# Optimization experiments

Hardware: AMD Instinct MI355X
Metric: run time of the kernel (lower is better)

The kernel has to match this reference:

```python
import jax, jax.numpy as jnp
import numpy as np

N, E, G = 100000, 1600000, 128
IN, HID, HEADS, EDIM, OUT = 16, 32, 4, 8, 4
HC = HEADS * HID


def _p(k, shape):
    return jax.random.normal(k, shape, jnp.float32) * 0.1


def setup_inputs():
    key = jax.random.key(0)
    ks = list(jax.random.split(key, 24))
    nxt = iter(ks)
    d = dict(
        x=jax.random.normal(next(nxt), (N, IN), jnp.float32),
        edge_index=jax.random.randint(next(nxt), (2, E), 0, N),
        edge_attr=jax.random.normal(next(nxt), (E, EDIM), jnp.float32),
        batch=jnp.sort(jax.random.randint(next(nxt), (N,), 0, G)),
    )
    # conv1: in=IN -> heads*hid
    d['wl1'] = _p(next(nxt), (IN, HC));  d['bl1'] = jnp.zeros((HC,), jnp.float32)
    d['wr1'] = _p(next(nxt), (IN, HC));  d['br1'] = jnp.zeros((HC,), jnp.float32)
    d['we1'] = _p(next(nxt), (EDIM, HC)); d['att1'] = _p(next(nxt), (HEADS, HID)); d['bc1'] = jnp.zeros((HC,), jnp.float32)
    # conv2: in=HC -> heads*hid
    d['wl2'] = _p(next(nxt), (HC, HC));  d['bl2'] = jnp.zeros((HC,), jnp.float32)
    d['wr2'] = _p(next(nxt), (HC, HC));  d['br2'] = jnp.zeros((HC,), jnp.float32)
    d['we2'] = _p(next(nxt), (EDIM, HC)); d['att2'] = _p(next(nxt), (HEADS, HID)); d['bc2'] = jnp.zeros((HC,), jnp.float32)
    # conv3: in=HC -> 1*hid (heads=1)
    d['wl3'] = _p(next(nxt), (HC, HID)); d['bl3'] = jnp.zeros((HID,), jnp.float32)
    d['wr3'] = _p(next(nxt), (HC, HID)); d['br3'] = jnp.zeros((HID,), jnp.float32)
    d['we3'] = _p(next(nxt), (EDIM, HID)); d['att3'] = _p(next(nxt), (1, HID)); d['bc3'] = jnp.zeros((HID,), jnp.float32)
    d['w_fc1'] = _p(next(nxt), (HID, 2 * HID)); d['b_fc1'] = jnp.zeros((2 * HID,), jnp.float32)
    d['w_fc2'] = _p(next(nxt), (2 * HID, OUT)); d['b_fc2'] = jnp.zeros((OUT,), jnp.float32)
    return d


def _gatv2(x, src, dst, eattr, wl, bl, wr, br, we, att, bias, n):
    # PyG GATv2Conv: e_ij = a^T . leaky_relu(Wl x_j + Wr x_i + We e_ij)
    H, C = att.shape
    xl = (x @ wl + bl).reshape(-1, H, C)  # source transform [N,H,C]
    xr = (x @ wr + br).reshape(-1, H, C)  # target transform [N,H,C]
    ea = (eattr @ we).reshape(-1, H, C)   # edge transform   [E,H,C]
    e = jax.nn.leaky_relu(xl[src] + xr[dst] + ea, 0.2)  # [E,H,C]
    logit = jnp.einsum('ehc,hc->eh', e, att)            # [E,H]
    m = jax.ops.segment_max(logit, dst, num_segments=n)
    p = jnp.exp(logit - m[dst])
    s = jax.ops.segment_sum(p, dst, num_segments=n)
    alpha = p / (s[dst] + 1e-16)                        # segment softmax per dst
    out = jax.ops.segment_sum(xl[src] * alpha[:, :, None], dst, num_segments=n)
    return out.reshape(n, H * C) + bias


def reference(x, edge_index, edge_attr, batch,
              wl1, bl1, wr1, br1, we1, att1, bc1,
              wl2, bl2, wr2, br2, we2, att2, bc2,
              wl3, bl3, wr3, br3, we3, att3, bc3,
              w_fc1, b_fc1, w_fc2, b_fc2):
    n = x.shape[0]
    src, dst = edge_index[0], edge_index[1]
    # add_self_loops=True with fill_value='mean' (mean of incoming edge_attr per node)
    ones_e = jnp.ones((src.shape[0],), x.dtype)
    cnt = jax.ops.segment_sum(ones_e, dst, num_segments=n)
    loop_attr = jax.ops.segment_sum(edge_attr, dst, num_segments=n) / jnp.maximum(cnt, 1.0)[:, None]
    ar = jnp.arange(n)
    src_a = jnp.concatenate([src, ar])
    dst_a = jnp.concatenate([dst, ar])
    ea = jnp.concatenate([edge_attr, loop_attr], axis=0)

    h = jax.nn.elu(_gatv2(x, src_a, dst_a, ea, wl1, bl1, wr1, br1, we1, att1, bc1, n))
    h = jax.nn.elu(_gatv2(h, src_a, dst_a, ea, wl2, bl2, wr2, br2, we2, att2, bc2, n))
    h = jax.nn.elu(_gatv2(h, src_a, dst_a, ea, wl3, bl3, wr3, br3, we3, att3, bc3, n))

    # global mean pool over graphs
    gs = jax.ops.segment_sum(h, batch, num_segments=G)
    gc = jax.ops.segment_sum(jnp.ones((n,), h.dtype), batch, num_segments=G)
    g = gs / jnp.maximum(gc, 1.0)[:, None]

    g = jax.nn.elu(g @ w_fc1 + b_fc1)
    return g @ w_fc2 + b_fc2
```

## Files before the change

### kernel.cpp

```cpp
#include <hip/hip_runtime.h>
#include <cstdint>
#include <type_traits>

constexpr int GNUM = 128;
constexpr int DBINS = 64;

typedef _Float16 h2 __attribute__((ext_vector_type(2)));
typedef _Float16 h4 __attribute__((ext_vector_type(4)));
typedef _Float16 h8 __attribute__((ext_vector_type(8)));
typedef float f4 __attribute__((ext_vector_type(4)));


__global__ __launch_bounds__(256) void hist_kernel(const int* __restrict__ dst,
                                                   int* __restrict__ cnt, int E) {
  int i = blockIdx.x * 256 + threadIdx.x;
  if (i < E) atomicAdd(&cnt[dst[i]], 1);
}

__global__ __launch_bounds__(256) void scan_part_kernel(const int* __restrict__ cnt,
                                                        int* __restrict__ bpart,
                                                        int* __restrict__ deghist, int n) {
  __shared__ int red[256];
  __shared__ int dh[DBINS];
  int base = blockIdx.x * 512;
  int t = threadIdx.x;
  if (t < DBINS) dh[t] = 0;
  __syncthreads();
  int s = 0;
  int i0 = base + t, i1 = base + 256 + t;
  if (i0 < n) { int c = cnt[i0] + 1; s += c; atomicAdd(&dh[c < DBINS - 1 ? c : DBINS - 1], 1); }
  if (i1 < n) { int c = cnt[i1] + 1; s += c; atomicAdd(&dh[c < DBINS - 1 ? c : DBINS - 1], 1); }
  red[t] = s;
  __syncthreads();
  for (int off = 128; off > 0; off >>= 1) {
    if (t < off) red[t] += red[t + off];
    __syncthreads();
  }
  if (t == 0) bpart[blockIdx.x] = red[0];
  if (t < DBINS && dh[t] > 0) atomicAdd(&deghist[t], dh[t]);
}

__global__ __launch_bounds__(1024) void scan_top_kernel(const int* __restrict__ bpart,
                                                        int* __restrict__ boff,
                                                        int* __restrict__ row_ptr,
                                                        const int* __restrict__ batch,
                                                        int* __restrict__ gstart,
                                                        const int* __restrict__ deghist,
                                                        int* __restrict__ degbase,
                                                        int B, int n) {
  __shared__ int buf[1024];
  __shared__ int dsc[DBINS];
  int t = threadIdx.x;
  buf[t] = (t < B) ? bpart[t] : 0;
  __syncthreads();
  for (int off = 1; off < 1024; off <<= 1) {
    int v = (t >= off) ? buf[t - off] : 0;
    __syncthreads();
    buf[t] += v;
    __syncthreads();
  }
  if (t < B) boff[t] = (t == 0) ? 0 : buf[t - 1];
  if (t == 0) row_ptr[n] = buf[1023];
  if (t <= GNUM) {
    int lo = 0, hi = n;
    while (lo < hi) {
      int mid = (lo + hi) >> 1;
      if (batch[mid] < t) lo = mid + 1; else hi = mid;
    }
    gstart[t] = lo;
  }
  int myc = 0;
  if (t < DBINS) { myc = deghist[t]; dsc[t] = myc; }
  __syncthreads();
  for (int off = 1; off < DBINS; off <<= 1) {
    int v = (t >= off && t < DBINS) ? dsc[t - off] : 0;
    __syncthreads();
    if (t < DBINS) dsc[t] += v;
    __syncthreads();
  }
  if (t < DBINS) degbase[t] = dsc[t] - myc;
}

__global__ __launch_bounds__(256) void scan_write_kernel(const int* __restrict__ cnt,
                                                         const int* __restrict__ boff,
                                                         int* __restrict__ row_ptr,
                                                         int* __restrict__ fill, int n) {
  __shared__ int red[256];
  int base = blockIdx.x * 512;
  int t = threadIdx.x;
  int i0 = base + 2 * t, i1 = base + 2 * t + 1;
  int v0 = (i0 < n) ? cnt[i0] + 1 : 0;
  int v1 = (i1 < n) ? cnt[i1] + 1 : 0;
  int val = v0 + v1;
  red[t] = val;
  __syncthreads();
  for (int off = 1; off < 256; off <<= 1) {
    int u = (t >= off) ? red[t - off] : 0;
    __syncthreads();
    red[t] += u;
    __syncthreads();
  }
  int o = boff[blockIdx.x] + red[t] - val;
  if (i0 < n) { row_ptr[i0] = o; fill[i0] = o; }
  if (i1 < n) { row_ptr[i1] = o + v0; fill[i1] = o + v0; }
}

__global__ __launch_bounds__(256) void permute_kernel(const int* __restrict__ cnt,
                                                      int* __restrict__ degbase,
                                                      int* __restrict__ perm, int n) {
  __shared__ int lcnt[DBINS];
  __shared__ int lbase[DBINS];
  int t = threadIdx.x;
  if (t < DBINS) lcnt[t] = 0;
  __syncthreads();
  int i = blockIdx.x * 256 + t;
  int bin = 0, lr = 0;
  if (i < n) {
    int c = cnt[i] + 1;
    bin = c < DBINS - 1 ? c : DBINS - 1;
    lr = atomicAdd(&lcnt[bin], 1);
  }
  __syncthreads();
  if (t < DBINS && lcnt[t] > 0) lbase[t] = atomicAdd(&degbase[t], lcnt[t]);
  __syncthreads();
  if (i < n) perm[lbase[bin] + lr] = i;
}

__global__ __launch_bounds__(256) void scatter_kernel(const int* __restrict__ src,
                                                      const int* __restrict__ dst,
                                                      const float* __restrict__ ea,
                                                      int* __restrict__ fill,
                                                      int* __restrict__ csr_src,
                                                      _Float16* __restrict__ ea_csr, int E) {
  int i = blockIdx.x * 256 + threadIdx.x;
  if (i >= E) return;
  int d = dst[i];
  int p = atomicAdd(&fill[d], 1);
  csr_src[p] = src[i];
  float4 e0 = *(const float4*)&ea[(size_t)i * 8];
  float4 e1 = *(const float4*)&ea[(size_t)i * 8 + 4];
  h8 v;
  v[0] = (_Float16)e0.x; v[1] = (_Float16)e0.y; v[2] = (_Float16)e0.z; v[3] = (_Float16)e0.w;
  v[4] = (_Float16)e1.x; v[5] = (_Float16)e1.y; v[6] = (_Float16)e1.z; v[7] = (_Float16)e1.w;
  *(h8*)&ea_csr[(size_t)p * 8] = v;
}

__global__ __launch_bounds__(256) void selfloop_kernel(const int* __restrict__ row_ptr,
                                                       int* __restrict__ csr_src,
                                                       _Float16* __restrict__ ea_csr, int n) {
  int idx = blockIdx.x * 256 + threadIdx.x;
  int i = idx >> 3, c = idx & 7;
  if (i >= n) return;
  int s = row_ptr[i], e = row_ptr[i + 1] - 1;
  float a = 0.f;
  for (int j = s; j < e; j++) a += (float)ea_csr[(size_t)j * 8 + c];
  float inv = 1.f / fmaxf((float)(e - s), 1.f);
  ea_csr[(size_t)e * 8 + c] = (_Float16)(a * inv);
  if (c == 0) csr_src[e] = i;
}

__global__ __launch_bounds__(256) void pack_all_kernel(
    const float* __restrict__ wl1, _Float16* __restrict__ p1l,
    const float* __restrict__ wr1, _Float16* __restrict__ p1r,
    const float* __restrict__ wl2, _Float16* __restrict__ p2l,
    const float* __restrict__ wr2, _Float16* __restrict__ p2r,
    const float* __restrict__ wl3, _Float16* __restrict__ p3l,
    const float* __restrict__ wr3, _Float16* __restrict__ p3r) {
  int y = blockIdx.y;
  const float* w; _Float16* wp; int Kreal, Kpad, NC;
  switch (y) {
    case 0: w = wl1; wp = p1l; Kreal = 16;  Kpad = 32;  NC = 128; break;
    case 1: w = wr1; wp = p1r; Kreal = 16;  Kpad = 32;  NC = 128; break;
    case 2: w = wl2; wp = p2l; Kreal = 128; Kpad = 128; NC = 128; break;
    case 3: w = wr2; wp = p2r; Kreal = 128; Kpad = 128; NC = 128; break;
    case 4: w = wl3; wp = p3l; Kreal = 128; Kpad = 128; NC = 32;  break;
    default: w = wr3; wp = p3r; Kreal = 128; Kpad = 128; NC = 32; break;
  }
  int KB = Kpad / 32;
  int total = (NC / 16) * KB * 64;
  int idx = blockIdx.x * 256 + threadIdx.x;
  if (idx >= total) return;
  int lane = idx & 63;
  int blk = idx >> 6;
  int nt = blk / KB, kb = blk % KB;
  int col = nt * 16 + (lane & 15);
  int krow = kb * 32 + (lane >> 4) * 8;
  h8 v;
#pragma unroll
  for (int j = 0; j < 8; j++)
    v[j] = (krow + j < Kreal) ? (_Float16)w[(size_t)(krow + j) * NC + col] : (_Float16)0.f;
  *(h8*)&wp[(size_t)idx * 8] = v;
}


template <int K, int NCOLS>
__global__ __launch_bounds__(256) void k1m_kernel(const _Float16* __restrict__ x,
                                                  const _Float16* __restrict__ wp0,
                                                  const float* __restrict__ b0,
                                                  _Float16* __restrict__ out0,
                                                  const _Float16* __restrict__ wp1,
                                                  const float* __restrict__ b1,
                                                  _Float16* __restrict__ out1, int n) {
  constexpr int NT = NCOLS / 16, KB = K / 32;
  const _Float16* wp = blockIdx.y ? wp1 : wp0;
  const float* b = blockIdx.y ? b1 : b0;
  _Float16* out = blockIdx.y ? out1 : out0;

  int tid = threadIdx.x;
  int wave = tid >> 6, lane = tid & 63;
  int m = lane & 15, quad = lane >> 4;
  int node0 = blockIdx.x * 64 + wave * 16;

  h8 afrag[KB];
  int anode = node0 + m;
  if (anode < n) {
#pragma unroll
    for (int kb = 0; kb < KB; kb++)
      afrag[kb] = *(const h8*)&x[(size_t)anode * K + kb * 32 + quad * 8];
  } else {
#pragma unroll
    for (int kb = 0; kb < KB; kb++) afrag[kb] = (h8)(_Float16)0.f;
  }

  f4 acc[NT] = {};
#pragma unroll
  for (int nt = 0; nt < NT; nt++) {
#pragma unroll
    for (int kb = 0; kb < KB; kb++) {
      h8 bfrag = *(const h8*)&wp[((size_t)(nt * KB + kb) * 64 + lane) * 8];
      acc[nt] = __builtin_amdgcn_mfma_f32_16x16x32_f16(afrag[kb], bfrag, acc[nt], 0, 0, 0);
    }
  }

#pragma unroll
  for (int nt = 0; nt < NT; nt++) {
#pragma unroll
    for (int r = 0; r < 4; r++) {
      int row = node0 + quad * 4 + r;
      if (row < n) {
        int col = nt * 16 + m;
        out[(size_t)row * NCOLS + col] = (_Float16)(acc[nt][r] + b[col]);
      }
    }
  }
}

template <int NCOLS>
__global__ __launch_bounds__(256) void k1m16_kernel(const float* __restrict__ x,
                                                    const _Float16* __restrict__ wp0,
                                                    const float* __restrict__ b0,
                                                    _Float16* __restrict__ out0,
                                                    const _Float16* __restrict__ wp1,
                                                    const float* __restrict__ b1,
                                                    _Float16* __restrict__ out1, int n) {
  constexpr int NT = NCOLS / 16;
  const _Float16* wp = blockIdx.y ? wp1 : wp0;
  const float* b = blockIdx.y ? b1 : b0;
  _Float16* out = blockIdx.y ? out1 : out0;

  int tid = threadIdx.x;
  int wave = tid >> 6, lane = tid & 63;
  int m = lane & 15, quad = lane >> 4;
  int node0 = blockIdx.x * 64 + wave * 16;

  int anode = node0 + m;
  h8 afrag = (h8)(_Float16)0.f;
  if (anode < n && quad < 2) {
    float4 v0 = *(const float4*)&x[(size_t)anode * 16 + quad * 8];
    float4 v1 = *(const float4*)&x[(size_t)anode * 16 + quad * 8 + 4];
    afrag[0] = (_Float16)v0.x; afrag[1] = (_Float16)v0.y;
    afrag[2] = (_Float16)v0.z; afrag[3] = (_Float16)v0.w;
    afrag[4] = (_Float16)v1.x; afrag[5] = (_Float16)v1.y;
    afrag[6] = (_Float16)v1.z; afrag[7] = (_Float16)v1.w;
  }

  f4 acc[NT] = {};
#pragma unroll
  for (int nt = 0; nt < NT; nt++) {
    h8 bfrag = *(const h8*)&wp[((size_t)nt * 64 + lane) * 8];
    acc[nt] = __builtin_amdgcn_mfma_f32_16x16x32_f16(afrag, bfrag, acc[nt], 0, 0, 0);
  }

#pragma unroll
  for (int nt = 0; nt < NT; nt++) {
#pragma unroll
    for (int r = 0; r < 4; r++) {
      int row = node0 + quad * 4 + r;
      if (row < n) {
        int col = nt * 16 + m;
        out[(size_t)row * NCOLS + col] = (_Float16)(acc[nt][r] + b[col]);
      }
    }
  }
}

template <int H>
__global__ __launch_bounds__(128) void k2_kernel(
    const _Float16* __restrict__ xl, const _Float16* __restrict__ xr,
    const int* __restrict__ row_ptr, const int* __restrict__ csr_src,
    const _Float16* __restrict__ ea_csr, const int* __restrict__ perm,
    const float* __restrict__ we, const float* __restrict__ att,
    const float* __restrict__ bc, _Float16* __restrict__ out, int n) {
  constexpr int HC = H * 32;
  constexpr int NL = HC / 4;
  constexpr int NPB = 128 / NL;

  int tid = threadIdx.x;
  int ln = tid / NL, q = tid % NL;
  int c0 = 4 * q;
  int nidx = blockIdx.x * NPB + ln;
  if (nidx >= n) return;
  int node = perm[nidx];

  h2 w2[8][2];
#pragma unroll
  for (int k = 0; k < 8; k++) {
    float4 v = *(const float4*)&we[k * HC + c0];
    w2[k][0] = h2{(_Float16)v.x, (_Float16)v.y};
    w2[k][1] = h2{(_Float16)v.z, (_Float16)v.w};
  }
  const float LOG2E = 1.44269504088896f;
  float4 av = *(const float4*)&att[c0];
  h2 a0 = h2{(_Float16)(av.x * LOG2E), (_Float16)(av.y * LOG2E)};
  h2 a1 = h2{(_Float16)(av.z * LOG2E), (_Float16)(av.w * LOG2E)};
  h4 xrh = *(const h4*)&xr[(size_t)node * HC + c0];
  h2 xr0 = h2{xrh[0], xrh[1]}, xr1 = h2{xrh[2], xrh[3]};
  const h2 p2 = h2{(_Float16)0.2f, (_Float16)0.2f};

  float acc[4] = {0.f, 0.f, 0.f, 0.f};
  float s = 0.f;

  int start = row_ptr[node], end = row_ptr[node + 1];
  int len = end - start;
  int pairs = (len + 1) >> 1;

  int j1 = (start + 1 < end) ? start + 1 : start;
  float m1 = (start + 1 < end) ? 1.f : 0.f;
  int s0 = csr_src[start], s1 = csr_src[j1];
  h8 e0 = *(const h8*)&ea_csr[(size_t)start * 8];
  h8 e1 = *(const h8*)&ea_csr[(size_t)j1 * 8];
  h4 x0 = *(const h4*)&xl[(size_t)s0 * HC + c0];
  h4 x1 = *(const h4*)&xl[(size_t)s1 * HC + c0];

#pragma unroll 2
  for (int p = 0; p < pairs; p++) {
    int jn = start + 2 * (p + 1);
    int k0 = (jn < end) ? jn : start;
    int k1 = (jn + 1 < end) ? jn + 1 : k0;
    float nm1 = (jn + 1 < end) ? 1.f : 0.f;
    int ns0 = csr_src[k0], ns1 = csr_src[k1];
    h8 ne0 = *(const h8*)&ea_csr[(size_t)k0 * 8];
    h8 ne1 = *(const h8*)&ea_csr[(size_t)k1 * 8];

    h2 t00 = h2{x0[0], x0[1]} + xr0;
    h2 t01 = h2{x0[2], x0[3]} + xr1;
    h2 t10 = h2{x1[0], x1[1]} + xr0;
    h2 t11 = h2{x1[2], x1[3]} + xr1;
#pragma unroll
    for (int k = 0; k < 8; k++) {
      h2 ev0 = h2{e0[k], e0[k]};
      h2 ev1 = h2{e1[k], e1[k]};
      t00 += ev0 * w2[k][0];
      t01 += ev0 * w2[k][1];
      t10 += ev1 * w2[k][0];
      t11 += ev1 * w2[k][1];
    }
    t00 = __builtin_elementwise_max(t00, t00 * p2);
    t01 = __builtin_elementwise_max(t01, t01 * p2);
    t10 = __builtin_elementwise_max(t10, t10 * p2);
    t11 = __builtin_elementwise_max(t11, t11 * p2);
    h2 pd0 = t00 * a0 + t01 * a1;
    h2 pd1 = t10 * a0 + t11 * a1;
    h2 pp = h2{(_Float16)(pd0[0] + pd0[1]), (_Float16)(pd1[0] + pd1[1])};

    h4 nx0 = *(const h4*)&xl[(size_t)ns0 * HC + c0];
    h4 nx1 = *(const h4*)&xl[(size_t)ns1 * HC + c0];

#pragma unroll
    for (int mseg = 1; mseg <= 4; mseg <<= 1) {
      int pv = __shfl_xor(__builtin_bit_cast(int, pp), mseg, 64);
      pp += __builtin_bit_cast(h2, pv);
    }
    float pe0 = __builtin_amdgcn_exp2f((float)pp[0]);
    float pe1 = __builtin_amdgcn_exp2f((float)pp[1]) * m1;
    s += pe0 + pe1;
#pragma unroll
    for (int i = 0; i < 4; i++)
      acc[i] += pe0 * (float)x0[i] + pe1 * (float)x1[i];

    s0 = ns0; s1 = ns1; e0 = ne0; e1 = ne1; x0 = nx0; x1 = nx1; m1 = nm1;
  }

  float inv = 1.f / (s + 1e-16f);
  h4 o;
#pragma unroll
  for (int i = 0; i < 4; i++) {
    float v = acc[i] * inv + bc[c0 + i];
    o[i] = (_Float16)(v > 0.f ? v : (__expf(v) - 1.f));
  }
  *(h4*)&out[(size_t)node * HC + c0] = o;
}

__global__ __launch_bounds__(256) void poolfc_kernel(const _Float16* __restrict__ h,
                                                     const int* __restrict__ gstart,
                                                     const float* __restrict__ w1,
                                                     const float* __restrict__ b1,
                                                     const float* __restrict__ w2,
                                                     const float* __restrict__ b2,
                                                     float* __restrict__ out) {
  __shared__ float red[256];
  __shared__ float g[32];
  __shared__ float a1[64];
  int gi = blockIdx.x;
  int t = threadIdx.x;
  int s = gstart[gi], e = gstart[gi + 1];
  int c = t & 31, rg = t >> 5;
  float acc = 0.f;
  for (int i = s + rg; i < e; i += 8) acc += (float)h[(size_t)i * 32 + c];
  red[t] = acc;
  __syncthreads();
  if (t < 128) red[t] += red[t + 128];
  __syncthreads();
  if (t < 64) red[t] += red[t + 64];
  __syncthreads();
  if (t < 32) g[t] = (red[t] + red[t + 32]) / fmaxf((float)(e - s), 1.f);
  __syncthreads();
  if (t < 64) {
    float v = b1[t];
    for (int k = 0; k < 32; k++) v += g[k] * w1[k * 64 + t];
    a1[t] = v > 0.f ? v : (__expf(v) - 1.f);
  }
  __syncthreads();
  if (t < 4) {
    float o = b2[t];
    for (int k = 0; k < 64; k++) o += a1[k] * w2[k * 4 + t];
    out[gi * 4 + t] = o;
  }
}


extern "C" void kernel_launch(void* const* d_in, const int* in_sizes, int n_in,
                              void* d_out, int out_size, void* d_ws, size_t ws_size,
                              hipStream_t stream) {
  const float* x     = (const float*)d_in[0];
  const int*   ei    = (const int*)d_in[1];
  const float* eattr = (const float*)d_in[2];
  const int*   batch = (const int*)d_in[3];
  const float *wl1 = (const float*)d_in[4],  *bl1 = (const float*)d_in[5];
  const float *wr1 = (const float*)d_in[6],  *br1 = (const float*)d_in[7];
  const float *we1 = (const float*)d_in[8],  *at1 = (const float*)d_in[9];
  const float *bc1 = (const float*)d_in[10];
  const float *wl2 = (const float*)d_in[11], *bl2 = (const float*)d_in[12];
  const float *wr2 = (const float*)d_in[13], *br2 = (const float*)d_in[14];
  const float *we2 = (const float*)d_in[15], *at2 = (const float*)d_in[16];
  const float *bc2 = (const float*)d_in[17];
  const float *wl3 = (const float*)d_in[18], *bl3 = (const float*)d_in[19];
  const float *wr3 = (const float*)d_in[20], *br3 = (const float*)d_in[21];
  const float *we3 = (const float*)d_in[22], *at3 = (const float*)d_in[23];
  const float *bc3 = (const float*)d_in[24];
  const float *wf1 = (const float*)d_in[25], *bf1 = (const float*)d_in[26];
  const float *wf2 = (const float*)d_in[27], *bf2 = (const float*)d_in[28];

  int N = in_sizes[0] / 16;
  int E = in_sizes[1] / 2;
  const int* srcp = ei;
  const int* dstp = ei + E;
  int EA = E + N;
  int NB = (N + 511) / 512;

  char* wsb = (char*)d_ws;
  size_t off = 0;
  auto alloc = [&](size_t bytes) -> char* {
    char* p = wsb + off;
    off += (bytes + 255) & ~(size_t)255;
    return p;
  };
  int*       cnt     = (int*)alloc((size_t)N * 4 + 2 * DBINS * 4);
  int*       deghist = cnt + N;
  int*       degbase = cnt + N + DBINS;
  int*       row_ptr = (int*)alloc((size_t)(N + 1) * 4);
  int*       fill    = (int*)alloc((size_t)N * 4);
  int*       bpart   = (int*)alloc((size_t)1024 * 4);
  int*       boff    = (int*)alloc((size_t)1024 * 4);
  int*       perm    = (int*)alloc((size_t)N * 4);
  int*       csr_src = (int*)alloc((size_t)EA * 4);
  _Float16*  ea_csr  = (_Float16*)alloc((size_t)EA * 8 * 2);
  _Float16*  xl      = (_Float16*)alloc((size_t)N * 128 * 2);
  _Float16*  xr      = (_Float16*)alloc((size_t)N * 128 * 2);
  _Float16*  h16     = (_Float16*)alloc((size_t)N * 128 * 2);
  _Float16*  h3      = (_Float16*)alloc((size_t)N * 32 * 2);
  int*       gstart  = (int*)alloc((size_t)(GNUM + 1) * 4);
  _Float16*  wp1l    = (_Float16*)alloc((size_t)32 * 128 * 2);
  _Float16*  wp1r    = (_Float16*)alloc((size_t)32 * 128 * 2);
  _Float16*  wp2l    = (_Float16*)alloc((size_t)128 * 128 * 2);
  _Float16*  wp2r    = (_Float16*)alloc((size_t)128 * 128 * 2);
  _Float16*  wp3l    = (_Float16*)alloc((size_t)128 * 32 * 2);
  _Float16*  wp3r    = (_Float16*)alloc((size_t)128 * 32 * 2);

  hipMemsetAsync(cnt, 0, (size_t)N * 4 + 2 * DBINS * 4, stream);

  hist_kernel<<<(E + 255) / 256, 256, 0, stream>>>(dstp, cnt, E);
  scan_part_kernel<<<NB, 256, 0, stream>>>(cnt, bpart, deghist, N);
  scan_top_kernel<<<1, 1024, 0, stream>>>(bpart, boff, row_ptr, batch, gstart,
                                          deghist, degbase, NB, N);
  scan_write_kernel<<<NB, 256, 0, stream>>>(cnt, boff, row_ptr, fill, N);
  permute_kernel<<<(N + 255) / 256, 256, 0, stream>>>(cnt, degbase, perm, N);
  scatter_kernel<<<(E + 255) / 256, 256, 0, stream>>>(srcp, dstp, eattr, fill, csr_src, ea_csr, E);
  selfloop_kernel<<<(N * 8 + 255) / 256, 256, 0, stream>>>(row_ptr, csr_src, ea_csr, N);
  pack_all_kernel<<<dim3(8, 6), 256, 0, stream>>>(wl1, wp1l, wr1, wp1r,
                                                  wl2, wp2l, wr2, wp2r,
                                                  wl3, wp3l, wr3, wp3r);

  k1m16_kernel<128><<<dim3((N + 63) / 64, 2), 256, 0, stream>>>(
      x, wp1l, bl1, xl, wp1r, br1, xr, N);
  k2_kernel<4><<<(N + 3) / 4, 128, 0, stream>>>(xl, xr, row_ptr, csr_src, ea_csr,
                                                perm, we1, at1, bc1, h16, N);
  k1m_kernel<128, 128><<<dim3((N + 63) / 64, 2), 256, 0, stream>>>(
      h16, wp2l, bl2, xl, wp2r, br2, xr, N);
  k2_kernel<4><<<(N + 3) / 4, 128, 0, stream>>>(xl, xr, row_ptr, csr_src, ea_csr,
                                                perm, we2, at2, bc2, h16, N);
  k1m_kernel<128, 32><<<dim3((N + 63) / 64, 2), 256, 0, stream>>>(
      h16, wp3l, bl3, xl, wp3r, br3, xr, N);
  k2_kernel<1><<<(N + 15) / 16, 128, 0, stream>>>(xl, xr, row_ptr, csr_src, ea_csr,
                                                  perm, we3, at3, bc3, h3, N);

  poolfc_kernel<<<GNUM, 256, 0, stream>>>(h3, gstart, wf1, bf1, wf2, bf2, (float*)d_out);
}
```

Measured before the change: 702.0 us.

## Split edge-attr scatter into index scatter plus coalesced gather, fuse permute into scan

The CSR build now scatters only edge ids, and a separate kernel gathers and converts each edge's attributes in CSR order, so the fp16 writes become coalesced while the reads are random. The degree-bucket permute kernel is folded into scan_write, which saves one launch. The self-loop mean kernel now has 8 lanes share a node's edges, loads whole 16-byte attribute rows and reduces them with shuffles, instead of strided per-channel reads. This adds an extra E-sized index array and one more kernel launch.

```diff
diff --git a/kernel.cpp b/kernel.cpp
--- a/kernel.cpp
+++ b/kernel.cpp
@@ -84,10 +84,16 @@
 __global__ __launch_bounds__(256) void scan_write_kernel(const int* __restrict__ cnt,
                                                          const int* __restrict__ boff,
                                                          int* __restrict__ row_ptr,
-                                                         int* __restrict__ fill, int n) {
+                                                         int* __restrict__ fill,
+                                                         int* __restrict__ degbase,
+                                                         int* __restrict__ perm,
+                                                         int* __restrict__ csr_eid, int n) {
   __shared__ int red[256];
+  __shared__ int lcnt[DBINS];
+  __shared__ int lbase[DBINS];
   int base = blockIdx.x * 512;
   int t = threadIdx.x;
+  if (t < DBINS) lcnt[t] = 0;
   int i0 = base + 2 * t, i1 = base + 2 * t + 1;
   int v0 = (i0 < n) ? cnt[i0] + 1 : 0;
   int v1 = (i1 < n) ? cnt[i1] + 1 : 0;
@@ -101,44 +107,41 @@
     __syncthreads();
   }
   int o = boff[blockIdx.x] + red[t] - val;
-  if (i0 < n) { row_ptr[i0] = o; fill[i0] = o; }
-  if (i1 < n) { row_ptr[i1] = o + v0; fill[i1] = o + v0; }
-}
-
-__global__ __launch_bounds__(256) void permute_kernel(const int* __restrict__ cnt,
-                                                      int* __restrict__ degbase,
-                                                      int* __restrict__ perm, int n) {
-  __shared__ int lcnt[DBINS];
-  __shared__ int lbase[DBINS];
-  int t = threadIdx.x;
-  if (t < DBINS) lcnt[t] = 0;
-  __syncthreads();
-  int i = blockIdx.x * 256 + t;
-  int bin = 0, lr = 0;
-  if (i < n) {
-    int c = cnt[i] + 1;
-    bin = c < DBINS - 1 ? c : DBINS - 1;
-    lr = atomicAdd(&lcnt[bin], 1);
-  }
+  if (i0 < n) { row_ptr[i0] = o; fill[i0] = o; csr_eid[o + v0 - 1] = -1; }
+  if (i1 < n) { row_ptr[i1] = o + v0; fill[i1] = o + v0; csr_eid[o + v0 + v1 - 1] = -1; }
+  int bin0 = 0, lr0 = 0, bin1 = 0, lr1 = 0;
+  if (i0 < n) { bin0 = v0 < DBINS - 1 ? v0 : DBINS - 1; lr0 = atomicAdd(&lcnt[bin0], 1); }
+  if (i1 < n) { bin1 = v1 < DBINS - 1 ? v1 : DBINS - 1; lr1 = atomicAdd(&lcnt[bin1], 1); }
   __syncthreads();
   if (t < DBINS && lcnt[t] > 0) lbase[t] = atomicAdd(&degbase[t], lcnt[t]);
   __syncthreads();
-  if (i < n) perm[lbase[bin] + lr] = i;
+  if (i0 < n) perm[lbase[bin0] + lr0] = i0;
+  if (i1 < n) perm[lbase[bin1] + lr1] = i1;
 }
 
 __global__ __launch_bounds__(256) void scatter_kernel(const int* __restrict__ src,
                                                       const int* __restrict__ dst,
-                                                      const float* __restrict__ ea,
                                                       int* __restrict__ fill,
                                                       int* __restrict__ csr_src,
-                                                      _Float16* __restrict__ ea_csr, int E) {
+                                                      int* __restrict__ csr_eid, int E) {
   int i = blockIdx.x * 256 + threadIdx.x;
   if (i >= E) return;
   int d = dst[i];
   int p = atomicAdd(&fill[d], 1);
   csr_src[p] = src[i];
-  float4 e0 = *(const float4*)&ea[(size_t)i * 8];
-  float4 e1 = *(const float4*)&ea[(size_t)i * 8 + 4];
+  csr_eid[p] = i;
+}
+
+__global__ __launch_bounds__(256) void gather_ea_kernel(const int* __restrict__ csr_eid,
+                                                        const float* __restrict__ ea,
+                                                        _Float16* __restrict__ ea_csr,
+                                                        int total) {
+  int p = blockIdx.x * 256 + threadIdx.x;
+  if (p >= total) return;
+  int eid = csr_eid[p];
+  if (eid < 0) return;
+  float4 e0 = *(const float4*)&ea[(size_t)eid * 8];
+  float4 e1 = *(const float4*)&ea[(size_t)eid * 8 + 4];
   h8 v;
   v[0] = (_Float16)e0.x; v[1] = (_Float16)e0.y; v[2] = (_Float16)e0.z; v[3] = (_Float16)e0.w;
   v[4] = (_Float16)e1.x; v[5] = (_Float16)e1.y; v[6] = (_Float16)e1.z; v[7] = (_Float16)e1.w;
@@ -152,11 +155,25 @@
   int i = idx >> 3, c = idx & 7;
   if (i >= n) return;
   int s = row_ptr[i], e = row_ptr[i + 1] - 1;
-  float a = 0.f;
-  for (int j = s; j < e; j++) a += (float)ea_csr[(size_t)j * 8 + c];
-  float inv = 1.f / fmaxf((float)(e - s), 1.f);
-  ea_csr[(size_t)e * 8 + c] = (_Float16)(a * inv);
-  if (c == 0) csr_src[e] = i;
+  float a[8] = {0, 0, 0, 0, 0, 0, 0, 0};
+  for (int j = s + c; j < e; j += 8) {
+    h8 t = *(const h8*)&ea_csr[(size_t)j * 8];
+#pragma unroll
+    for (int k = 0; k < 8; k++) a[k] += (float)t[k];
+  }
+#pragma unroll
+  for (int off = 1; off <= 4; off <<= 1) {
+#pragma unroll
+    for (int k = 0; k < 8; k++) a[k] += __shfl_xor(a[k], off, 64);
+  }
+  if (c == 0) {
+    float inv = 1.f / fmaxf((float)(e - s), 1.f);
+    h8 o;
+#pragma unroll
+    for (int k = 0; k < 8; k++) o[k] = (_Float16)(a[k] * inv);
+    *(h8*)&ea_csr[(size_t)e * 8] = o;
+    csr_src[e] = i;
+  }
 }
 
 __global__ __launch_bounds__(256) void pack_all_kernel(
@@ -484,6 +501,7 @@
   int*       boff    = (int*)alloc((size_t)1024 * 4);
   int*       perm    = (int*)alloc((size_t)N * 4);
   int*       csr_src = (int*)alloc((size_t)EA * 4);
+  int*       csr_eid = (int*)alloc((size_t)EA * 4);
   _Float16*  ea_csr  = (_Float16*)alloc((size_t)EA * 8 * 2);
   _Float16*  xl      = (_Float16*)alloc((size_t)N * 128 * 2);
   _Float16*  xr      = (_Float16*)alloc((size_t)N * 128 * 2);
@@ -503,9 +521,10 @@
   scan_part_kernel<<<NB, 256, 0, stream>>>(cnt, bpart, deghist, N);
   scan_top_kernel<<<1, 1024, 0, stream>>>(bpart, boff, row_ptr, batch, gstart,
                                           deghist, degbase, NB, N);
-  scan_write_kernel<<<NB, 256, 0, stream>>>(cnt, boff, row_ptr, fill, N);
-  permute_kernel<<<(N + 255) / 256, 256, 0, stream>>>(cnt, degbase, perm, N);
-  scatter_kernel<<<(E + 255) / 256, 256, 0, stream>>>(srcp, dstp, eattr, fill, csr_src, ea_csr, E);
+  scan_write_kernel<<<NB, 256, 0, stream>>>(cnt, boff, row_ptr, fill, degbase,
+                                            perm, csr_eid, N);
+  scatter_kernel<<<(E + 255) / 256, 256, 0, stream>>>(srcp, dstp, fill, csr_src, csr_eid, E);
+  gather_ea_kernel<<<(EA + 255) / 256, 256, 0, stream>>>(csr_eid, eattr, ea_csr, EA);
   selfloop_kernel<<<(N * 8 + 255) / 256, 256, 0, stream>>>(row_ptr, csr_src, ea_csr, N);
   pack_all_kernel<<<dim3(8, 6), 256, 0, stream>>>(wl1, wp1l, wr1, wp1r,
                                                   wl2, wp2l, wr2, wp2r,
```

Result: slower. 734.4 us (+4.6%).
